# Kernel tuning notes

Measured on AMD Instinct MI355X. Metric: run time of the kernel, lower is better.

## Reference

```python
import jax, jax.numpy as jnp
import numpy as np

B, F, INP, S = 2048, 50, 2, 1024
LN_EPS = 1e-3
UPDATE_BIAS = -1.0
_TRUNC = 0.8796256610342398  # trunc-normal std correction from weight_init


def _std(fan_in, fan_out):
    return np.sqrt(2.0 / (fan_in + fan_out)) / _TRUNC


def setup_inputs() -> dict:
    key = jax.random.key(0)
    k_act, k_emb, k_gru, k_dec = jax.random.split(key, 4)
    return {
        "action": jax.random.normal(k_act, (B, F, INP), dtype=jnp.float32),
        "W_emb": jax.random.normal(k_emb, (INP, S), dtype=jnp.float32) * _std(INP, S),
        "W_gru": jax.random.normal(k_gru, (2 * S, 3 * S), dtype=jnp.float32) * _std(2 * S, 3 * S),
        "ln_gamma": jnp.ones((3 * S,), dtype=jnp.float32),
        "ln_beta": jnp.zeros((3 * S,), dtype=jnp.float32),
        "W_dec": jax.random.normal(k_dec, (S, INP), dtype=jnp.float32) * _std(S, INP),
        "b_dec": jnp.zeros((INP,), dtype=jnp.float32),
    }


def reference(action, W_emb, W_gru, ln_gamma, ln_beta, W_dec, b_dec):
    # action: [b, f, inp]
    emb = jnp.einsum("bfi,is->bfs", action, W_emb)  # [b, f, s]

    def step(prev, x_t):
        # prev, x_t: [b, s]
        parts = jnp.concatenate([x_t, prev], axis=-1) @ W_gru  # [b, 3s]
        mu = parts.mean(-1, keepdims=True)
        var = parts.var(-1, keepdims=True)
        parts = (parts - mu) / jnp.sqrt(var + LN_EPS) * ln_gamma + ln_beta
        reset, cand, update = jnp.split(parts, 3, axis=-1)
        reset = jax.nn.sigmoid(reset)
        cand = jnp.tanh(reset * cand)
        update = jax.nn.sigmoid(update + UPDATE_BIAS)
        h = update * cand + (1.0 - update) * prev
        return h, None

    prev0 = jnp.zeros_like(emb[:, 0])
    h_last, _ = jax.lax.scan(step, prev0, jnp.swapaxes(emb, 0, 1))  # scan over f
    outputs = h_last @ W_dec + b_dec  # [b, inp]
    return h_last[:, None], outputs[:, None]
```

## Files before the change

kernel.cpp:

```cpp
#include <hip/hip_runtime.h>

typedef unsigned short u16;
typedef unsigned int   u32;
typedef _Float16       f16;

#define B_SZ 2048
#define S_SZ 1024
#define N3   3072
#define F_SZ 50

typedef f16    f16x8 __attribute__((ext_vector_type(8)));
typedef f16    f16x4 __attribute__((ext_vector_type(4)));
typedef float  f32x4 __attribute__((ext_vector_type(4)));
typedef u32    u32x4 __attribute__((ext_vector_type(4)));

__device__ __forceinline__ void glds16(const void* g, void* l) {
    __builtin_amdgcn_global_load_lds(
        (const __attribute__((address_space(1))) u32*)g,
        (__attribute__((address_space(3))) u32*)l, 16, 0, 0);
}

__global__ __launch_bounds__(256) void make_mx(
    const float* __restrict__ We, const float* __restrict__ Wg,
    float* __restrict__ Mx)
{
    int j  = blockIdx.x * 256 + threadIdx.x;
    int k0 = blockIdx.y * 64;
    float s0 = 0.f, s1 = 0.f;
    #pragma unroll 4
    for (int k = k0; k < k0 + 64; k++) {
        float w = Wg[(size_t)k * N3 + j];
        s0 += We[k] * w;
        s1 += We[S_SZ + k] * w;
    }
    atomicAdd(&Mx[j], s0);
    atomicAdd(&Mx[N3 + j], s1);
}

__global__ __launch_bounds__(256) void transpose_w(
    const float* __restrict__ Wg, f16* __restrict__ Wt)
{
    __shared__ float tile[32][33];
    int n0 = blockIdx.x * 32, k0 = blockIdx.y * 32;
    int c = threadIdx.x & 31, r = threadIdx.x >> 5;
    #pragma unroll
    for (int s = 0; s < 4; s++) {
        int rr = r + s * 8;
        tile[rr][c] = Wg[(size_t)(S_SZ + k0 + rr) * N3 + n0 + c];
    }
    __syncthreads();
    #pragma unroll
    for (int s = 0; s < 4; s++) {
        int rr = r + s * 8;
        Wt[(size_t)(n0 + rr) * S_SZ + k0 + c] = (f16)tile[c][rr];
    }
}

__global__ __launch_bounds__(256) void gemm_step(
    const f16* __restrict__ Wt,
    const f16* __restrict__ hh,
    const float* __restrict__ Mx,
    const float* __restrict__ act,
    f16* __restrict__ parts,
    int t)
{
    __shared__ __align__(16) f16 As[64 * 64];
    __shared__ __align__(16) f16 Bs[128 * 64];
    const int m0 = blockIdx.x * 64;
    const int n0 = blockIdx.y * 128;
    const int tid  = threadIdx.x;
    const int lane = tid & 63;
    const int wave = tid >> 6;
    const int wr = (wave >> 1) * 32;
    const int wc = (wave & 1) * 64;
    const int quad = lane >> 4, lrow = lane & 15;
    const int swz = (lrow & 7) * 8;

    const int lrow8 = lane >> 3;
    const int scolh = ((lane & 7) * 8) ^ (lrow8 * 8);

    f32x4 acc[2][4];
    #pragma unroll
    for (int i = 0; i < 2; i++)
        #pragma unroll
        for (int j = 0; j < 4; j++)
            acc[i][j] = (f32x4){0.f, 0.f, 0.f, 0.f};

    for (int kb = 0; kb < S_SZ; kb += 64) {
        __syncthreads();
        #pragma unroll
        for (int c = 0; c < 2; c++) {
            int ch = wave * 2 + c;
            int row = ch * 8 + lrow8;
            glds16(&hh[(size_t)(m0 + row) * S_SZ + kb + scolh], &As[ch * 512]);
        }
        #pragma unroll
        for (int c = 0; c < 4; c++) {
            int ch = wave * 4 + c;
            int row = ch * 8 + lrow8;
            glds16(&Wt[(size_t)(n0 + row) * S_SZ + kb + scolh], &Bs[ch * 512]);
        }
        __syncthreads();
        #pragma unroll
        for (int kk = 0; kk < 64; kk += 32) {
            f16x8 a[2], b[4];
            #pragma unroll
            for (int i = 0; i < 2; i++)
                a[i] = __builtin_bit_cast(f16x8,
                    *(const u32x4*)&As[(wr + i * 16 + lrow) * 64 +
                                       ((kk + quad * 8) ^ swz)]);
            #pragma unroll
            for (int j = 0; j < 4; j++)
                b[j] = __builtin_bit_cast(f16x8,
                    *(const u32x4*)&Bs[(wc + j * 16 + lrow) * 64 +
                                       ((kk + quad * 8) ^ swz)]);
            #pragma unroll
            for (int i = 0; i < 2; i++)
                #pragma unroll
                for (int j = 0; j < 4; j++)
                    acc[i][j] = __builtin_amdgcn_mfma_f32_16x16x32_f16(
                        a[i], b[j], acc[i][j], 0, 0, 0);
        }
    }

    #pragma unroll
    for (int i = 0; i < 2; i++) {
        #pragma unroll
        for (int rr = 0; rr < 4; rr++) {
            int m = m0 + wr + i * 16 + quad * 4 + rr;
            float a0 = act[((size_t)m * F_SZ + t) * 2 + 0];
            float a1 = act[((size_t)m * F_SZ + t) * 2 + 1];
            #pragma unroll
            for (int j = 0; j < 4; j++) {
                int n = n0 + wc + j * 16 + lrow;
                parts[(size_t)m * N3 + n] =
                    (f16)(acc[i][j][rr] + a0 * Mx[n] + a1 * Mx[N3 + n]);
            }
        }
    }
}

__global__ __launch_bounds__(256) void ln_gate_step(
    const f16* __restrict__ parts,
    const float* __restrict__ gamma,
    const float* __restrict__ beta,
    f16* __restrict__ hh,
    float* __restrict__ hout,
    int t)
{
    const int tid = threadIdx.x;
    const int r2  = tid >> 7;
    const int tl  = tid & 127;
    const int row = blockIdx.x * 2 + r2;
    const f16* p = parts + (size_t)row * N3 + tl * 8;

    float v[24];
    float s = 0.f, ss = 0.f;
    #pragma unroll
    for (int g = 0; g < 3; g++) {
        f16x8 x = *(const f16x8*)(p + g * S_SZ);
        #pragma unroll
        for (int e = 0; e < 8; e++) {
            float f = (float)x[e];
            v[g * 8 + e] = f;
            s += f; ss += f * f;
        }
    }
    #pragma unroll
    for (int o = 1; o < 64; o <<= 1) {
        s  += __shfl_xor(s, o);
        ss += __shfl_xor(ss, o);
    }
    __shared__ float red[8];
    int wave = tid >> 6, lane = tid & 63;
    if (lane == 0) { red[wave] = s; red[4 + wave] = ss; }
    __syncthreads();
    float S  = red[r2 * 2] + red[r2 * 2 + 1];
    float SS = red[4 + r2 * 2] + red[4 + r2 * 2 + 1];
    float mean = S * (1.f / N3);
    float var  = SS * (1.f / N3) - mean * mean;
    float rstd = rsqrtf(var + 1e-3f);

    float nv[24];
    #pragma unroll
    for (int g = 0; g < 3; g++) {
        f32x4 g0 = *(const f32x4*)(gamma + g * S_SZ + tl * 8);
        f32x4 g1 = *(const f32x4*)(gamma + g * S_SZ + tl * 8 + 4);
        f32x4 b0 = *(const f32x4*)(beta  + g * S_SZ + tl * 8);
        f32x4 b1 = *(const f32x4*)(beta  + g * S_SZ + tl * 8 + 4);
        #pragma unroll
        for (int e = 0; e < 4; e++) {
            nv[g * 8 + e]     = (v[g * 8 + e]     - mean) * rstd * g0[e] + b0[e];
            nv[g * 8 + e + 4] = (v[g * 8 + e + 4] - mean) * rstd * g1[e] + b1[e];
        }
    }

    size_t hbase = (size_t)row * S_SZ + tl * 8;
    f16x8 hp = *(const f16x8*)(hh + hbase);
    f16x8 hs;
    f32x4 ho0, ho1;
    #pragma unroll
    for (int e = 0; e < 8; e++) {
        float rg = 1.f / (1.f + __expf(-nv[e]));
        float x  = rg * nv[8 + e];
        float tt = __expf(-2.f * fabsf(x));
        float cg = __builtin_copysignf((1.f - tt) / (1.f + tt), x);
        float ug = 1.f / (1.f + __expf(-(nv[16 + e] - 1.f)));
        float hv = ug * cg + (1.f - ug) * (float)hp[e];
        hs[e] = (f16)hv;
        if (e < 4) ho0[e] = hv; else ho1[e - 4] = hv;
    }
    *(f16x8*)(hh + hbase) = hs;
    if (t == F_SZ - 1) {
        *(f32x4*)(hout + hbase)     = ho0;
        *(f32x4*)(hout + hbase + 4) = ho1;
    }
}

__global__ __launch_bounds__(256) void final_out(
    const float* __restrict__ h, const float* __restrict__ Wd,
    const float* __restrict__ bd, float* __restrict__ out)
{
    int row = blockIdx.x * 4 + (threadIdx.x >> 6);
    int lane = threadIdx.x & 63;
    const float* hr = h + (size_t)row * S_SZ;
    float s0 = 0.f, s1 = 0.f;
    #pragma unroll
    for (int k = lane; k < S_SZ; k += 64) {
        float x = hr[k];
        s0 += x * Wd[k * 2];
        s1 += x * Wd[k * 2 + 1];
    }
    #pragma unroll
    for (int o = 32; o > 0; o >>= 1) {
        s0 += __shfl_down(s0, o);
        s1 += __shfl_down(s1, o);
    }
    if (lane == 0) {
        out[(size_t)B_SZ * S_SZ + row * 2 + 0] = s0 + bd[0];
        out[(size_t)B_SZ * S_SZ + row * 2 + 1] = s1 + bd[1];
    }
}

extern "C" void kernel_launch(void* const* d_in, const int* in_sizes, int n_in,
                              void* d_out, int out_size, void* d_ws, size_t ws_size,
                              hipStream_t stream)
{
    const float* act = (const float*)d_in[0];
    const float* We  = (const float*)d_in[1];
    const float* Wg  = (const float*)d_in[2];
    const float* lng = (const float*)d_in[3];
    const float* lnb = (const float*)d_in[4];
    const float* Wd  = (const float*)d_in[5];
    const float* bd  = (const float*)d_in[6];
    float* out = (float*)d_out;

    char* ws = (char*)d_ws;
    f16*   Wt    = (f16*)ws;
    float* Mx    = (float*)(ws + 6291456);
    f16*   hh    = (f16*)(ws + 6316032);
    f16*   parts = (f16*)(ws + 10510336);

    hipMemsetAsync(hh, 0, (size_t)B_SZ * S_SZ * 2, stream);
    hipMemsetAsync(Mx, 0, 2 * N3 * 4, stream);
    make_mx<<<dim3(N3 / 256, 16), 256, 0, stream>>>(We, Wg, Mx);
    transpose_w<<<dim3(N3 / 32, S_SZ / 32), 256, 0, stream>>>(Wg, Wt);

    for (int t = 0; t < F_SZ; t++) {
        gemm_step<<<dim3(32, 24), 256, 0, stream>>>(Wt, hh, Mx, act, parts, t);
        ln_gate_step<<<B_SZ / 2, 256, 0, stream>>>(parts, lng, lnb, hh, out, t);
    }
    final_out<<<B_SZ / 4, 256, 0, stream>>>(out, Wd, bd, out);
}
```

Measured before the change: 1.492 ms.

## Triple-buffer GEMM step with larger 128x192 tiles and one block per CU

```diff
diff --git a/kernel.cpp b/kernel.cpp
--- a/kernel.cpp
+++ b/kernel.cpp
@@ -10,7 +10,6 @@
 #define F_SZ 50
 
 typedef f16    f16x8 __attribute__((ext_vector_type(8)));
-typedef f16    f16x4 __attribute__((ext_vector_type(4)));
 typedef float  f32x4 __attribute__((ext_vector_type(4)));
 typedef u32    u32x4 __attribute__((ext_vector_type(4)));
 
@@ -56,7 +55,12 @@
     }
 }
 
-__global__ __launch_bounds__(256) void gemm_step(
+#define BM 128
+#define BN 192
+#define BK 64
+#define NT (S_SZ / BK)
+
+__global__ __launch_bounds__(512) void gemm_step(
     const f16* __restrict__ Wt,
     const f16* __restrict__ hh,
     const float* __restrict__ Mx,
@@ -64,77 +68,128 @@
     f16* __restrict__ parts,
     int t)
 {
-    __shared__ __align__(16) f16 As[64 * 64];
-    __shared__ __align__(16) f16 Bs[128 * 64];
-    const int m0 = blockIdx.x * 64;
-    const int n0 = blockIdx.y * 128;
+    __shared__ __align__(16) f16 As[3][BM * BK];
+    __shared__ __align__(16) f16 Bs[3][BN * BK];
+
+    const int bid = blockIdx.x;
+    const int wid = (bid & 7) * 32 + (bid >> 3);
+    const int mt  = wid & 15, nt = wid >> 4;
+    const int m0  = mt * BM, n0 = nt * BN;
+
     const int tid  = threadIdx.x;
     const int lane = tid & 63;
     const int wave = tid >> 6;
-    const int wr = (wave >> 1) * 32;
-    const int wc = (wave & 1) * 64;
+    const int wm   = wave >> 2;
+    const int wn   = wave & 3;
+    const int wr   = wm * 64;
+    const int wc   = wn * 48;
     const int quad = lane >> 4, lrow = lane & 15;
-    const int swz = (lrow & 7) * 8;
+    const int swz  = (lrow & 7) * 8;
 
     const int lrow8 = lane >> 3;
     const int scolh = ((lane & 7) * 8) ^ (lrow8 * 8);
 
-    f32x4 acc[2][4];
-    #pragma unroll
-    for (int i = 0; i < 2; i++)
-        #pragma unroll
-        for (int j = 0; j < 4; j++)
+    f32x4 acc[4][3];
+    #pragma unroll
+    for (int i = 0; i < 4; i++)
+        #pragma unroll
+        for (int j = 0; j < 3; j++)
             acc[i][j] = (f32x4){0.f, 0.f, 0.f, 0.f};
 
-    for (int kb = 0; kb < S_SZ; kb += 64) {
-        __syncthreads();
+    auto stage = [&](int kt, int buf) {
+        const int kb = kt * BK;
         #pragma unroll
         for (int c = 0; c < 2; c++) {
-            int ch = wave * 2 + c;
+            int ch  = wave * 2 + c;
             int row = ch * 8 + lrow8;
-            glds16(&hh[(size_t)(m0 + row) * S_SZ + kb + scolh], &As[ch * 512]);
-        }
-        #pragma unroll
-        for (int c = 0; c < 4; c++) {
-            int ch = wave * 4 + c;
+            glds16(&hh[(size_t)(m0 + row) * S_SZ + kb + scolh],
+                   &As[buf][ch * 512]);
+        }
+        #pragma unroll
+        for (int c = 0; c < 3; c++) {
+            int ch  = wave * 3 + c;
             int row = ch * 8 + lrow8;
-            glds16(&Wt[(size_t)(n0 + row) * S_SZ + kb + scolh], &Bs[ch * 512]);
-        }
-        __syncthreads();
-        #pragma unroll
-        for (int kk = 0; kk < 64; kk += 32) {
-            f16x8 a[2], b[4];
+            glds16(&Wt[(size_t)(n0 + row) * S_SZ + kb + scolh],
+                   &Bs[buf][ch * 512]);
+        }
+    };
+
+    stage(0, 0);
+    stage(1, 1);
+    asm volatile("s_waitcnt vmcnt(5)" ::: "memory");
+    __builtin_amdgcn_s_barrier();
+
+    for (int kt = 0; kt < NT; ++kt) {
+        const int rb = kt % 3;
+        const f16* Ab = As[rb];
+        const f16* Bb = Bs[rb];
+
+        f16x8 a[4], b[3];
+        #pragma unroll
+        for (int i = 0; i < 4; i++)
+            a[i] = __builtin_bit_cast(f16x8,
+                *(const u32x4*)&Ab[(wr + i * 16 + lrow) * BK +
+                                   ((quad * 8) ^ swz)]);
+        #pragma unroll
+        for (int j = 0; j < 3; j++)
+            b[j] = __builtin_bit_cast(f16x8,
+                *(const u32x4*)&Bb[(wc + j * 16 + lrow) * BK +
+                                   ((quad * 8) ^ swz)]);
+        if (kt < NT - 2) stage(kt + 2, (kt + 2) % 3);
+        __builtin_amdgcn_s_barrier();
+        __builtin_amdgcn_s_setprio(1);
+        #pragma unroll
+        for (int i = 0; i < 4; i++)
             #pragma unroll
-            for (int i = 0; i < 2; i++)
-                a[i] = __builtin_bit_cast(f16x8,
-                    *(const u32x4*)&As[(wr + i * 16 + lrow) * 64 +
-                                       ((kk + quad * 8) ^ swz)]);
+            for (int j = 0; j < 3; j++)
+                acc[i][j] = __builtin_amdgcn_mfma_f32_16x16x32_f16(
+                    a[i], b[j], acc[i][j], 0, 0, 0);
+        __builtin_amdgcn_s_setprio(0);
+        __builtin_amdgcn_s_barrier();
+
+        #pragma unroll
+        for (int i = 0; i < 4; i++)
+            a[i] = __builtin_bit_cast(f16x8,
+                *(const u32x4*)&Ab[(wr + i * 16 + lrow) * BK +
+                                   ((32 + quad * 8) ^ swz)]);
+        #pragma unroll
+        for (int j = 0; j < 3; j++)
+            b[j] = __builtin_bit_cast(f16x8,
+                *(const u32x4*)&Bb[(wc + j * 16 + lrow) * BK +
+                                   ((32 + quad * 8) ^ swz)]);
+        if (kt < NT - 2) asm volatile("s_waitcnt vmcnt(5)" ::: "memory");
+        else             asm volatile("s_waitcnt vmcnt(0)" ::: "memory");
+        __builtin_amdgcn_s_barrier();
+        __builtin_amdgcn_s_setprio(1);
+        #pragma unroll
+        for (int i = 0; i < 4; i++)
             #pragma unroll
-            for (int j = 0; j < 4; j++)
-                b[j] = __builtin_bit_cast(f16x8,
-                    *(const u32x4*)&Bs[(wc + j * 16 + lrow) * 64 +
-                                       ((kk + quad * 8) ^ swz)]);
-            #pragma unroll
-            for (int i = 0; i < 2; i++)
-                #pragma unroll
-                for (int j = 0; j < 4; j++)
-                    acc[i][j] = __builtin_amdgcn_mfma_f32_16x16x32_f16(
-                        a[i], b[j], acc[i][j], 0, 0, 0);
-        }
-    }
-
-    #pragma unroll
-    for (int i = 0; i < 2; i++) {
+            for (int j = 0; j < 3; j++)
+                acc[i][j] = __builtin_amdgcn_mfma_f32_16x16x32_f16(
+                    a[i], b[j], acc[i][j], 0, 0, 0);
+        __builtin_amdgcn_s_setprio(0);
+        __builtin_amdgcn_s_barrier();
+    }
+
+    float mx0[3], mx1[3];
+    #pragma unroll
+    for (int j = 0; j < 3; j++) {
+        int n = n0 + wc + j * 16 + lrow;
+        mx0[j] = Mx[n];
+        mx1[j] = Mx[N3 + n];
+    }
+    #pragma unroll
+    for (int i = 0; i < 4; i++) {
         #pragma unroll
         for (int rr = 0; rr < 4; rr++) {
             int m = m0 + wr + i * 16 + quad * 4 + rr;
             float a0 = act[((size_t)m * F_SZ + t) * 2 + 0];
             float a1 = act[((size_t)m * F_SZ + t) * 2 + 1];
             #pragma unroll
-            for (int j = 0; j < 4; j++) {
+            for (int j = 0; j < 3; j++) {
                 int n = n0 + wc + j * 16 + lrow;
                 parts[(size_t)m * N3 + n] =
-                    (f16)(acc[i][j][rr] + a0 * Mx[n] + a1 * Mx[N3 + n]);
+                    (f16)(acc[i][j][rr] + a0 * mx0[j] + a1 * mx1[j]);
             }
         }
     }
@@ -267,7 +322,7 @@
     transpose_w<<<dim3(N3 / 32, S_SZ / 32), 256, 0, stream>>>(Wg, Wt);
 
     for (int t = 0; t < F_SZ; t++) {
-        gemm_step<<<dim3(32, 24), 256, 0, stream>>>(Wt, hh, Mx, act, parts, t);
+        gemm_step<<<dim3(256), dim3(512), 0, stream>>>(Wt, hh, Mx, act, parts, t);
         ln_gate_step<<<B_SZ / 2, 256, 0, stream>>>(parts, lng, lnb, hh, out, t);
     }
     final_out<<<B_SZ / 4, 256, 0, stream>>>(out, Wd, bd, out);
```

Result: slower. 1.608 ms (+7.8%).

## Retile per-step GEMM to 128x96 blocks with XCD-aware block mapping

Applied to the files above, without the earlier changes.

```diff
diff --git a/kernel.cpp b/kernel.cpp
--- a/kernel.cpp
+++ b/kernel.cpp
@@ -10,7 +10,6 @@
 #define F_SZ 50
 
 typedef f16    f16x8 __attribute__((ext_vector_type(8)));
-typedef f16    f16x4 __attribute__((ext_vector_type(4)));
 typedef float  f32x4 __attribute__((ext_vector_type(4)));
 typedef u32    u32x4 __attribute__((ext_vector_type(4)));
 
@@ -56,7 +55,11 @@
     }
 }
 
-__global__ __launch_bounds__(256) void gemm_step(
+#define BM 128
+#define BN 96
+#define BK 64
+
+__global__ __launch_bounds__(256, 2) void gemm_step(
     const f16* __restrict__ Wt,
     const f16* __restrict__ hh,
     const float* __restrict__ Mx,
@@ -64,77 +67,90 @@
     f16* __restrict__ parts,
     int t)
 {
-    __shared__ __align__(16) f16 As[64 * 64];
-    __shared__ __align__(16) f16 Bs[128 * 64];
-    const int m0 = blockIdx.x * 64;
-    const int n0 = blockIdx.y * 128;
+    __shared__ __align__(16) f16 As[BM * BK];
+    __shared__ __align__(16) f16 Bs[BN * BK];
+
+    const int bid = blockIdx.x;
+    const int xcd = bid & 7;
+    const int loc = bid >> 3;
+    const int mt  = (xcd & 1) * 8 + (loc & 7);
+    const int nt  = (xcd >> 1) * 8 + (loc >> 3);
+    const int m0  = mt * BM, n0 = nt * BN;
+
     const int tid  = threadIdx.x;
     const int lane = tid & 63;
     const int wave = tid >> 6;
-    const int wr = (wave >> 1) * 32;
-    const int wc = (wave & 1) * 64;
+    const int wr   = (wave >> 1) * 64;
+    const int wc   = (wave & 1) * 48;
     const int quad = lane >> 4, lrow = lane & 15;
-    const int swz = (lrow & 7) * 8;
+    const int swz  = (lrow & 7) * 8;
 
     const int lrow8 = lane >> 3;
     const int scolh = ((lane & 7) * 8) ^ (lrow8 * 8);
 
-    f32x4 acc[2][4];
-    #pragma unroll
-    for (int i = 0; i < 2; i++)
-        #pragma unroll
-        for (int j = 0; j < 4; j++)
+    f32x4 acc[4][3];
+    #pragma unroll
+    for (int i = 0; i < 4; i++)
+        #pragma unroll
+        for (int j = 0; j < 3; j++)
             acc[i][j] = (f32x4){0.f, 0.f, 0.f, 0.f};
 
-    for (int kb = 0; kb < S_SZ; kb += 64) {
+    for (int kb = 0; kb < S_SZ; kb += BK) {
         __syncthreads();
         #pragma unroll
-        for (int c = 0; c < 2; c++) {
-            int ch = wave * 2 + c;
+        for (int c = 0; c < 4; c++) {
+            int ch  = wave * 4 + c;
             int row = ch * 8 + lrow8;
             glds16(&hh[(size_t)(m0 + row) * S_SZ + kb + scolh], &As[ch * 512]);
         }
         #pragma unroll
-        for (int c = 0; c < 4; c++) {
-            int ch = wave * 4 + c;
+        for (int c = 0; c < 3; c++) {
+            int ch  = wave * 3 + c;
             int row = ch * 8 + lrow8;
             glds16(&Wt[(size_t)(n0 + row) * S_SZ + kb + scolh], &Bs[ch * 512]);
         }
         __syncthreads();
         #pragma unroll
         for (int kk = 0; kk < 64; kk += 32) {
-            f16x8 a[2], b[4];
-            #pragma unroll
-            for (int i = 0; i < 2; i++)
+            f16x8 a[4], b[3];
+            #pragma unroll
+            for (int i = 0; i < 4; i++)
                 a[i] = __builtin_bit_cast(f16x8,
                     *(const u32x4*)&As[(wr + i * 16 + lrow) * 64 +
                                        ((kk + quad * 8) ^ swz)]);
             #pragma unroll
-            for (int j = 0; j < 4; j++)
+            for (int j = 0; j < 3; j++)
                 b[j] = __builtin_bit_cast(f16x8,
                     *(const u32x4*)&Bs[(wc + j * 16 + lrow) * 64 +
                                        ((kk + quad * 8) ^ swz)]);
             #pragma unroll
-            for (int i = 0; i < 2; i++)
+            for (int i = 0; i < 4; i++)
                 #pragma unroll
-                for (int j = 0; j < 4; j++)
+                for (int j = 0; j < 3; j++)
                     acc[i][j] = __builtin_amdgcn_mfma_f32_16x16x32_f16(
                         a[i], b[j], acc[i][j], 0, 0, 0);
         }
     }
 
-    #pragma unroll
-    for (int i = 0; i < 2; i++) {
+    float mx0[3], mx1[3];
+    #pragma unroll
+    for (int j = 0; j < 3; j++) {
+        int n = n0 + wc + j * 16 + lrow;
+        mx0[j] = Mx[n];
+        mx1[j] = Mx[N3 + n];
+    }
+    #pragma unroll
+    for (int i = 0; i < 4; i++) {
         #pragma unroll
         for (int rr = 0; rr < 4; rr++) {
             int m = m0 + wr + i * 16 + quad * 4 + rr;
             float a0 = act[((size_t)m * F_SZ + t) * 2 + 0];
             float a1 = act[((size_t)m * F_SZ + t) * 2 + 1];
             #pragma unroll
-            for (int j = 0; j < 4; j++) {
+            for (int j = 0; j < 3; j++) {
                 int n = n0 + wc + j * 16 + lrow;
                 parts[(size_t)m * N3 + n] =
-                    (f16)(acc[i][j][rr] + a0 * Mx[n] + a1 * Mx[N3 + n]);
+                    (f16)(acc[i][j][rr] + a0 * mx0[j] + a1 * mx1[j]);
             }
         }
     }
@@ -267,7 +283,7 @@
     transpose_w<<<dim3(N3 / 32, S_SZ / 32), 256, 0, stream>>>(Wg, Wt);
 
     for (int t = 0; t < F_SZ; t++) {
-        gemm_step<<<dim3(32, 24), 256, 0, stream>>>(Wt, hh, Mx, act, parts, t);
+        gemm_step<<<dim3(512), 256, 0, stream>>>(Wt, hh, Mx, act, parts, t);
         ln_gate_step<<<B_SZ / 2, 256, 0, stream>>>(parts, lng, lnb, hh, out, t);
     }
     final_out<<<B_SZ / 4, 256, 0, stream>>>(out, Wd, bd, out);
```

Result: slower. 1.559 ms (+4.5%).

## Store hidden state in MFMA fragment layout and load A operands directly from global

Applied to the files above, without the earlier changes.

```diff
diff --git a/kernel.cpp b/kernel.cpp
--- a/kernel.cpp
+++ b/kernel.cpp
@@ -8,9 +8,9 @@
 #define S_SZ 1024
 #define N3   3072
 #define F_SZ 50
+#define NK   32
 
 typedef f16    f16x8 __attribute__((ext_vector_type(8)));
-typedef f16    f16x4 __attribute__((ext_vector_type(4)));
 typedef float  f32x4 __attribute__((ext_vector_type(4)));
 typedef u32    u32x4 __attribute__((ext_vector_type(4)));
 
@@ -19,6 +19,7 @@
         (const __attribute__((address_space(1))) u32*)g,
         (__attribute__((address_space(3))) u32*)l, 16, 0, 0);
 }
+
 
 __global__ __launch_bounds__(256) void make_mx(
     const float* __restrict__ We, const float* __restrict__ Wg,
@@ -58,13 +59,12 @@
 
 __global__ __launch_bounds__(256) void gemm_step(
     const f16* __restrict__ Wt,
-    const f16* __restrict__ hh,
+    const f16* __restrict__ hhF,
     const float* __restrict__ Mx,
     const float* __restrict__ act,
     f16* __restrict__ parts,
     int t)
 {
-    __shared__ __align__(16) f16 As[64 * 64];
     __shared__ __align__(16) f16 Bs[128 * 64];
     const int m0 = blockIdx.x * 64;
     const int n0 = blockIdx.y * 128;
@@ -79,6 +79,9 @@
     const int lrow8 = lane >> 3;
     const int scolh = ((lane & 7) * 8) ^ (lrow8 * 8);
 
+    const int R0 = (m0 + wr) >> 4;
+    const f16* Ab = hhF + (size_t)R0 * NK * 512 + lane * 8;
+
     f32x4 acc[2][4];
     #pragma unroll
     for (int i = 0; i < 2; i++)
@@ -88,27 +91,25 @@
 
     for (int kb = 0; kb < S_SZ; kb += 64) {
         __syncthreads();
-        #pragma unroll
-        for (int c = 0; c < 2; c++) {
-            int ch = wave * 2 + c;
-            int row = ch * 8 + lrow8;
-            glds16(&hh[(size_t)(m0 + row) * S_SZ + kb + scolh], &As[ch * 512]);
-        }
         #pragma unroll
         for (int c = 0; c < 4; c++) {
             int ch = wave * 4 + c;
             int row = ch * 8 + lrow8;
             glds16(&Wt[(size_t)(n0 + row) * S_SZ + kb + scolh], &Bs[ch * 512]);
         }
+        const int kb32 = kb >> 5;
+        f16x8 a0[2], a1[2];
+        #pragma unroll
+        for (int i = 0; i < 2; i++) {
+            a0[i] = __builtin_bit_cast(f16x8,
+                *(const u32x4*)(Ab + (((size_t)i * NK + kb32) << 9)));
+            a1[i] = __builtin_bit_cast(f16x8,
+                *(const u32x4*)(Ab + (((size_t)i * NK + kb32 + 1) << 9)));
+        }
         __syncthreads();
         #pragma unroll
         for (int kk = 0; kk < 64; kk += 32) {
-            f16x8 a[2], b[4];
-            #pragma unroll
-            for (int i = 0; i < 2; i++)
-                a[i] = __builtin_bit_cast(f16x8,
-                    *(const u32x4*)&As[(wr + i * 16 + lrow) * 64 +
-                                       ((kk + quad * 8) ^ swz)]);
+            f16x8 b[4];
             #pragma unroll
             for (int j = 0; j < 4; j++)
                 b[j] = __builtin_bit_cast(f16x8,
@@ -119,7 +120,7 @@
                 #pragma unroll
                 for (int j = 0; j < 4; j++)
                     acc[i][j] = __builtin_amdgcn_mfma_f32_16x16x32_f16(
-                        a[i], b[j], acc[i][j], 0, 0, 0);
+                        (kk == 0) ? a0[i] : a1[i], b[j], acc[i][j], 0, 0, 0);
         }
     }
 
@@ -195,8 +196,9 @@
         }
     }
 
-    size_t hbase = (size_t)row * S_SZ + tl * 8;
-    f16x8 hp = *(const f16x8*)(hh + hbase);
+    size_t hfrag = ((size_t)(row >> 4) * NK + (tl >> 2)) * 512
+                 + ((size_t)((tl & 3) * 16 + (row & 15))) * 8;
+    f16x8 hp = *(const f16x8*)(hh + hfrag);
     f16x8 hs;
     f32x4 ho0, ho1;
     #pragma unroll
@@ -210,8 +212,9 @@
         hs[e] = (f16)hv;
         if (e < 4) ho0[e] = hv; else ho1[e - 4] = hv;
     }
-    *(f16x8*)(hh + hbase) = hs;
+    *(f16x8*)(hh + hfrag) = hs;
     if (t == F_SZ - 1) {
+        size_t hbase = (size_t)row * S_SZ + tl * 8;
         *(f32x4*)(hout + hbase)     = ho0;
         *(f32x4*)(hout + hbase + 4) = ho1;
     }
```

After: 1.859 ms. 24.6% more time.
